# Kernel tuning notes

Measured on AMD Instinct MI355X. Metric: run time of the kernel, lower is better.

The kernel has to match this reference:

```python
import jax, jax.numpy as jnp
import numpy as np

EPS = 1e-5
THRESH = 1.5


def _compute_one(x, g_w, g_b, phi_w, phi_b, W_w, W_b, gamma, beta):
    # x: (c, w, h, z) -- single sample (torch code calls compute_x with batch 1)
    c, w, h, z = x.shape
    nz = z // 2
    # AdaptiveAvgPool3d(1) on x.permute(0,4,2,3,1): mean over (w, h, c) per z-slice -> (z,)
    p = x.mean(axis=(0, 1, 2))
    xp = x * p[None, None, None, :]
    # 1x1x1 conv projections (note: self.theta is defined but unused in the original)
    g_x = jnp.einsum('ic,cwhz->iwhz', g_w, x) + g_b[:, None, None, None]
    phi_x = jnp.einsum('ic,cwhz->iwhz', phi_w, xp) + phi_b[:, None, None, None]
    # MaxPool3d kernel (1,1,2): non-overlapping max pairs along z
    g_x = g_x.reshape(-1, w, h, nz, 2).max(axis=-1)      # (ic, w, h, nz)
    phi_x = phi_x.reshape(-1, w, h, nz, 2).max(axis=-1)  # (ic, w, h, nz)
    # theta_x: (x*p).permute(0,2,3,4,1).view(w*h, z, c)
    theta = xp.transpose(1, 2, 3, 0).reshape(w * h, z, c)
    # phi: permute(0,2,3,1,4).view(w*h, ic, nz)
    phi_m = phi_x.transpose(1, 2, 0, 3).reshape(w * h, -1, nz)
    # g: permute(0,2,3,4,1).view(w*h, nz, ic)
    g_m = g_x.transpose(1, 2, 3, 0).reshape(w * h, nz, -1)
    f = jnp.einsum('bzc,bcn->bzn', theta, phi_m)          # (wh, z, nz)
    a = jax.nn.softmax(f, axis=-1)
    y = jnp.einsum('bzn,bni->bzi', a, g_m)                # (wh, z, ic)
    y = y.reshape(w, h, z, -1).transpose(3, 0, 1, 2)      # (ic, w, h, z)
    wy = jnp.einsum('ci,iwhz->cwhz', W_w, y) + W_b[:, None, None, None]
    # BatchNorm3d in training mode on a single-sample batch: per-channel stats over (w,h,z)
    mu = wy.mean(axis=(1, 2, 3), keepdims=True)
    var = wy.var(axis=(1, 2, 3), keepdims=True)
    wy = (wy - mu) * jax.lax.rsqrt(var + EPS)
    wy = wy * gamma[:, None, None, None] + beta[:, None, None, None]
    return wy + x


def setup_inputs() -> dict:
    key = jax.random.key(0)
    ks = jax.random.split(key, 10)
    b, c, w, h, z = 2, 64, 64, 64, 64
    ic = c  # inter_channels defaults to in_channels
    x = jax.random.normal(ks[0], (b, c, w, h, z), dtype=jnp.float32)
    # spacings in [0, 3): some samples fall above spacing_thresh=1.5 (identity branch)
    spacings = jax.random.uniform(ks[1], (b, 3), dtype=jnp.float32) * 3.0
    g_w = jax.random.normal(ks[2], (ic, c), dtype=jnp.float32) * 0.1
    g_b = jax.random.normal(ks[3], (ic,), dtype=jnp.float32) * 0.1
    phi_w = jax.random.normal(ks[4], (ic, c), dtype=jnp.float32) * 0.1
    phi_b = jax.random.normal(ks[5], (ic,), dtype=jnp.float32) * 0.1
    W_w = jax.random.normal(ks[6], (c, ic), dtype=jnp.float32) * 0.1
    W_b = jax.random.normal(ks[7], (c,), dtype=jnp.float32) * 0.1
    gamma = jax.random.normal(ks[8], (c,), dtype=jnp.float32) * 0.1
    beta = jax.random.normal(ks[9], (c,), dtype=jnp.float32) * 0.1
    return {"x": x, "spacings": spacings, "g_w": g_w, "g_b": g_b,
            "phi_w": phi_w, "phi_b": phi_b, "W_w": W_w, "W_b": W_b,
            "gamma": gamma, "beta": beta}


def reference(x, spacings, g_w, g_b, phi_w, phi_b, W_w, W_b, gamma, beta):
    out = jax.vmap(_compute_one, in_axes=(0,) + (None,) * 8)(
        x, g_w, g_b, phi_w, phi_b, W_w, W_b, gamma, beta)
    use = (spacings[:, -1] <= THRESH)[:, None, None, None, None]
    return jnp.where(use, out, x)
```

## Files before the change

kernel.cpp:

```cpp
#include <hip/hip_runtime.h>
#include <math.h>

#define THRESH_SP 1.5f
#define WHZc   262144
#define CWHZc  16777216

#define WS_PSUM   0
#define WS_SLOT   128
#define WS_SC     8320
#define WS_SH     8448
#define WS_ZERO_N 8320

typedef __attribute__((ext_vector_type(8))) short bf16x8;
typedef __attribute__((ext_vector_type(4))) float floatx4;

#define MFMA(a, b, c) __builtin_amdgcn_mfma_f32_16x16x32_bf16((a), (b), (c), 0, 0, 0)

__device__ __forceinline__ unsigned short f2b(float f) {
    unsigned int u = __builtin_bit_cast(unsigned int, f);
    return (unsigned short)((u + 0x7FFFu + ((u >> 16) & 1u)) >> 16);
}
__device__ __forceinline__ float b2f(unsigned short h) {
    unsigned int u = ((unsigned int)h) << 16;
    return __builtin_bit_cast(float, u);
}
__device__ __forceinline__ unsigned int scale2(unsigned int u, float pv) {
    unsigned short lo = f2b(b2f((unsigned short)(u & 0xffffu)) * pv);
    unsigned short hi = f2b(b2f((unsigned short)(u >> 16)) * pv);
    return (unsigned int)lo | ((unsigned int)hi << 16);
}
__device__ __forceinline__ bf16x8 ldfrag(const unsigned short* p, int elem_off) {
    return *(const bf16x8*)(p + elem_off);
}

__global__ __launch_bounds__(256) void k_zero(float* __restrict__ ws) {
    int i = blockIdx.x * blockDim.x + threadIdx.x;
    if (i < WS_ZERO_N) ws[i] = 0.0f;
}

__global__ __launch_bounds__(256) void k_pmean(const float* __restrict__ x,
                                               const float* __restrict__ sp,
                                               float* __restrict__ ws) {
    const int b = blockIdx.x >> 9;
    if (sp[b*3 + 2] > THRESH_SP) return;
    const int jb = blockIdx.x & 511;
    __shared__ float s[64];
    const int t = threadIdx.x;
    if (t < 64) s[t] = 0.0f;
    __syncthreads();
    const int idx4 = jb * 256 + t;
    const int z0 = (idx4 & 15) * 4;
    float a0 = 0.f, a1 = 0.f, a2 = 0.f, a3 = 0.f;
    const float* xb = x + (size_t)b * CWHZc;
#pragma unroll 4
    for (int it = 0; it < 32; ++it) {
        const float4 v = *(const float4*)&xb[(size_t)(idx4 + it * 131072) * 4];
        a0 += v.x; a1 += v.y; a2 += v.z; a3 += v.w;
    }
    a0 += __shfl_xor(a0, 16); a0 += __shfl_xor(a0, 32);
    a1 += __shfl_xor(a1, 16); a1 += __shfl_xor(a1, 32);
    a2 += __shfl_xor(a2, 16); a2 += __shfl_xor(a2, 32);
    a3 += __shfl_xor(a3, 16); a3 += __shfl_xor(a3, 32);
    if ((t & 63) < 16) {
        unsafeAtomicAdd(&s[z0 + 0], a0);
        unsafeAtomicAdd(&s[z0 + 1], a1);
        unsafeAtomicAdd(&s[z0 + 2], a2);
        unsafeAtomicAdd(&s[z0 + 3], a3);
    }
    __syncthreads();
    if (t < 64) unsafeAtomicAdd(&ws[WS_PSUM + b * 64 + t], s[t]);
}

__global__ __launch_bounds__(256, 4) void k_main(
    const float* __restrict__ x, const float* __restrict__ sp,
    const float* __restrict__ gw, const float* __restrict__ gb,
    const float* __restrict__ pw, const float* __restrict__ pb,
    const float* __restrict__ Wwp, const float* __restrict__ Wbp,
    float* __restrict__ out, float* __restrict__ ws) {
    const int blk = blockIdx.x;
    const int b = blk >> 12;
    if (sp[b*3 + 2] > THRESH_SP) return;
    const int wh = blk & 4095;
    const int xbase = b * CWHZc + wh * 64;

    __shared__ unsigned short xT[64 * 72];
    __shared__ unsigned short wb[64 * 72];
    __shared__ unsigned short gpT[64 * 40];
    __shared__ unsigned short phpN[32 * 72];
    __shared__ unsigned short aT[64 * 40];
    __shared__ float p_s[64];

    const int t  = threadIdx.x;
    const int l  = t & 63;
    const int lr = l & 15;
    const int lq = l >> 4;
    const int zt = (t >> 6) << 4;

#pragma unroll
    for (int k = 0; k < 4; ++k) {
        const int f = t + (k << 8);
        const int c = f & 63, zq = f >> 6;
        const float4 v = *(const float4*)&x[xbase + c * WHZc + zq * 4];
        xT[(zq*4 + 0)*72 + c] = f2b(v.x);
        xT[(zq*4 + 1)*72 + c] = f2b(v.y);
        xT[(zq*4 + 2)*72 + c] = f2b(v.z);
        xT[(zq*4 + 3)*72 + c] = f2b(v.w);
    }
#pragma unroll
    for (int k = 0; k < 4; ++k) {
        const int f = t + (k << 8);
        const int i = f >> 4, c4 = f & 15;
        const float4 v = *(const float4*)&gw[i*64 + c4*4];
        uint2 pk;
        pk.x = (unsigned int)f2b(v.x) | ((unsigned int)f2b(v.y) << 16);
        pk.y = (unsigned int)f2b(v.z) | ((unsigned int)f2b(v.w) << 16);
        *(uint2*)&wb[i*72 + c4*4] = pk;
    }
    if (t < 64) p_s[t] = ws[WS_PSUM + b*64 + t] * (1.0f / 262144.0f);
    __syncthreads();

    {
        const bf16x8 a0 = ldfrag(xT, (zt + lr)*72 + lq*8);
        const bf16x8 a1 = ldfrag(xT, (zt + lr)*72 + lq*8 + 32);
        const int n0 = (zt >> 1) + lq*2;
#pragma unroll
        for (int ti = 0; ti < 4; ++ti) {
            const int i = ti*16 + lr;
            const float bv = gb[i];
            floatx4 acc = {bv, bv, bv, bv};
            acc = MFMA(a0, ldfrag(wb, i*72 + lq*8), acc);
            acc = MFMA(a1, ldfrag(wb, i*72 + lq*8 + 32), acc);
            unsigned int pk = (unsigned int)f2b(fmaxf(acc[0], acc[1])) |
                              ((unsigned int)f2b(fmaxf(acc[2], acc[3])) << 16);
            *(unsigned int*)&gpT[i*40 + n0] = pk;
        }
    }
    __syncthreads();

    {
        const int r = t & 63, cb = (t >> 6) * 2;
        const float pv = p_s[r];
#pragma unroll
        for (int cc = 0; cc < 2; ++cc) {
            uint4 q = *(uint4*)&xT[r*72 + (cb + cc)*8];
            q.x = scale2(q.x, pv); q.y = scale2(q.y, pv);
            q.z = scale2(q.z, pv); q.w = scale2(q.w, pv);
            *(uint4*)&xT[r*72 + (cb + cc)*8] = q;
        }
#pragma unroll
        for (int k = 0; k < 4; ++k) {
            const int f = t + (k << 8);
            const int i = f >> 4, c4 = f & 15;
            const float4 v = *(const float4*)&pw[i*64 + c4*4];
            uint2 pk;
            pk.x = (unsigned int)f2b(v.x) | ((unsigned int)f2b(v.y) << 16);
            pk.y = (unsigned int)f2b(v.z) | ((unsigned int)f2b(v.w) << 16);
            *(uint2*)&wb[i*72 + c4*4] = pk;
        }
    }
    __syncthreads();

    {
        const bf16x8 a0 = ldfrag(xT, (zt + lr)*72 + lq*8);
        const bf16x8 a1 = ldfrag(xT, (zt + lr)*72 + lq*8 + 32);
        const int n0 = (zt >> 1) + lq*2;
#pragma unroll
        for (int ti = 0; ti < 4; ++ti) {
            const int i = ti*16 + lr;
            const float bv = pb[i];
            floatx4 acc = {bv, bv, bv, bv};
            acc = MFMA(a0, ldfrag(wb, i*72 + lq*8), acc);
            acc = MFMA(a1, ldfrag(wb, i*72 + lq*8 + 32), acc);
            phpN[n0*72 + i]       = f2b(fmaxf(acc[0], acc[1]));
            phpN[(n0 + 1)*72 + i] = f2b(fmaxf(acc[2], acc[3]));
        }
    }
    __syncthreads();

    {
        const bf16x8 a0 = ldfrag(xT, (zt + lr)*72 + lq*8);
        const bf16x8 a1 = ldfrag(xT, (zt + lr)*72 + lq*8 + 32);
        floatx4 f0 = {0.f, 0.f, 0.f, 0.f}, f1 = {0.f, 0.f, 0.f, 0.f};
        f0 = MFMA(a0, ldfrag(phpN, lr*72 + lq*8), f0);
        f0 = MFMA(a1, ldfrag(phpN, lr*72 + lq*8 + 32), f0);
        f1 = MFMA(a0, ldfrag(phpN, (16 + lr)*72 + lq*8), f1);
        f1 = MFMA(a1, ldfrag(phpN, (16 + lr)*72 + lq*8 + 32), f1);
#pragma unroll
        for (int r = 0; r < 4; ++r) {
            float m = fmaxf(f0[r], f1[r]);
            m = fmaxf(m, __shfl_xor(m, 1)); m = fmaxf(m, __shfl_xor(m, 2));
            m = fmaxf(m, __shfl_xor(m, 4)); m = fmaxf(m, __shfl_xor(m, 8));
            const float e0 = __expf(f0[r] - m), e1 = __expf(f1[r] - m);
            float s = e0 + e1;
            s += __shfl_xor(s, 1); s += __shfl_xor(s, 2);
            s += __shfl_xor(s, 4); s += __shfl_xor(s, 8);
            const float inv = 1.0f / s;
            const int z = zt + lq*4 + r;
            aT[z*40 + lr]      = f2b(e0 * inv);
            aT[z*40 + lr + 16] = f2b(e1 * inv);
        }
#pragma unroll
        for (int k = 0; k < 4; ++k) {
            const int f = t + (k << 8);
            const int i = f >> 4, c4 = f & 15;
            const float4 v = *(const float4*)&Wwp[i*64 + c4*4];
            uint2 pk;
            pk.x = (unsigned int)f2b(v.x) | ((unsigned int)f2b(v.y) << 16);
            pk.y = (unsigned int)f2b(v.z) | ((unsigned int)f2b(v.w) << 16);
            *(uint2*)&wb[i*72 + c4*4] = pk;
        }
    }
    __syncthreads();

    {
        float* statsf = (float*)phpN;
        if (t < 128) statsf[t] = 0.0f;
        const bf16x8 av = ldfrag(aT, (zt + lr)*40 + lq*8);
#pragma unroll
        for (int ti = 0; ti < 4; ++ti) {
            floatx4 acc = {0.f, 0.f, 0.f, 0.f};
            acc = MFMA(av, ldfrag(gpT, (ti*16 + lr)*40 + lq*8), acc);
#pragma unroll
            for (int r = 0; r < 4; ++r)
                xT[(zt + lq*4 + r)*72 + ti*16 + lr] = f2b(acc[r]);
        }
    }
    __syncthreads();

    {
        float* statsf = (float*)phpN;
        const bf16x8 a0 = ldfrag(xT, (zt + lr)*72 + lq*8);
        const bf16x8 a1 = ldfrag(xT, (zt + lr)*72 + lq*8 + 32);
#pragma unroll
        for (int ti = 0; ti < 4; ++ti) {
            const int co = ti*16 + lr;
            const float bv = Wbp[co];
            floatx4 acc = {bv, bv, bv, bv};
            acc = MFMA(a0, ldfrag(wb, co*72 + lq*8), acc);
            acc = MFMA(a1, ldfrag(wb, co*72 + lq*8 + 32), acc);
            *(float4*)&out[xbase + co * WHZc + zt + lq*4] = *(float4*)&acc;
            float s1 = acc[0] + acc[1] + acc[2] + acc[3];
            float s2 = acc[0]*acc[0] + acc[1]*acc[1] + acc[2]*acc[2] + acc[3]*acc[3];
            s1 += __shfl_xor(s1, 16); s1 += __shfl_xor(s1, 32);
            s2 += __shfl_xor(s2, 16); s2 += __shfl_xor(s2, 32);
            if (lq == 0) {
                atomicAdd(&statsf[co*2],     s1);
                atomicAdd(&statsf[co*2 + 1], s2);
            }
        }
    }
    __syncthreads();
    {
        const float* statsf = (const float*)phpN;
        if (t < 128) {
            const int slot = blk & 31;
            unsafeAtomicAdd(&ws[WS_SLOT + (slot*2 + b)*128 + t], statsf[t]);
        }
    }
}

__global__ __launch_bounds__(128) void k_stats(const float* __restrict__ gamma,
                                               const float* __restrict__ beta,
                                               float* __restrict__ ws) {
    const int t = threadIdx.x;
    if (t >= 128) return;
    const int b = t >> 6, c = t & 63;
    float S1 = 0.f, S2 = 0.f;
    for (int s = 0; s < 32; s++) {
        S1 += ws[WS_SLOT + ((s * 2 + b) * 64 + c) * 2 + 0];
        S2 += ws[WS_SLOT + ((s * 2 + b) * 64 + c) * 2 + 1];
    }
    const float N = 262144.0f;
    const float mu = S1 / N;
    const float var = fmaxf(S2 / N - mu * mu, 0.0f);
    const float sc = gamma[c] * rsqrtf(var + 1e-5f);
    ws[WS_SC + t] = sc;
    ws[WS_SH + t] = beta[c] - mu * sc;
}

__global__ __launch_bounds__(256) void k_final(const float* __restrict__ x,
                                               const float* __restrict__ sp,
                                               float* __restrict__ out,
                                               const float* __restrict__ ws) {
    const bool use0 = sp[2] <= THRESH_SP;
    const bool use1 = sp[5] <= THRESH_SP;
    const int nf4 = (2 * CWHZc) / 4;
    for (int i4 = blockIdx.x * blockDim.x + threadIdx.x; i4 < nf4;
         i4 += gridDim.x * blockDim.x) {
        const int idx = i4 * 4;
        const int b = idx >> 24;
        const bool use = b ? use1 : use0;
        const float4 xv = *(const float4*)&x[idx];
        float4 ov;
        if (use) {
            const int c = (idx >> 18) & 63;
            const float scv = ws[WS_SC + b * 64 + c];
            const float shv = ws[WS_SH + b * 64 + c];
            const float4 wy = *(const float4*)&out[idx];
            ov.x = wy.x * scv + shv + xv.x;
            ov.y = wy.y * scv + shv + xv.y;
            ov.z = wy.z * scv + shv + xv.z;
            ov.w = wy.w * scv + shv + xv.w;
        } else {
            ov = xv;
        }
        *(float4*)&out[idx] = ov;
    }
}

extern "C" void kernel_launch(void* const* d_in, const int* in_sizes, int n_in,
                              void* d_out, int out_size, void* d_ws, size_t ws_size,
                              hipStream_t stream) {
    const float* x     = (const float*)d_in[0];
    const float* spv   = (const float*)d_in[1];
    const float* gw    = (const float*)d_in[2];
    const float* gb    = (const float*)d_in[3];
    const float* pw    = (const float*)d_in[4];
    const float* pb    = (const float*)d_in[5];
    const float* Ww    = (const float*)d_in[6];
    const float* Wb    = (const float*)d_in[7];
    const float* gamma = (const float*)d_in[8];
    const float* beta  = (const float*)d_in[9];
    float* out = (float*)d_out;
    float* ws  = (float*)d_ws;

    k_zero<<<(WS_ZERO_N + 255) / 256, 256, 0, stream>>>(ws);
    k_pmean<<<1024, 256, 0, stream>>>(x, spv, ws);
    k_main<<<8192, 256, 0, stream>>>(x, spv, gw, gb, pw, pb, Ww, Wb, out, ws);
    k_stats<<<1, 128, 0, stream>>>(gamma, beta, ws);
    k_final<<<2048, 256, 0, stream>>>(x, spv, out, ws);
}
```

Measured before the change: 136.4 us.

## Fold p-scaling into projections, store wy as bf16, merge stats into final kernel

The per-z scaling by p is no longer applied to the x tile in shared memory. It is folded algebraically into the phi projection output and the attention logits, which removes one pass over the tile and one barrier. When the workspace is large enough, the intermediate W·y result is written as bf16 to the workspace instead of fp32 to the output, halving that intermediate traffic at some precision cost. The separate k_stats launch is folded into k_final, where each block recomputes the BN scale and shift in shared memory, adding redundant per-block work in exchange for one fewer launch.

```diff
diff --git a/kernel.cpp b/kernel.cpp
--- a/kernel.cpp
+++ b/kernel.cpp
@@ -7,9 +7,9 @@
 
 #define WS_PSUM   0
 #define WS_SLOT   128
-#define WS_SC     8320
-#define WS_SH     8448
 #define WS_ZERO_N 8320
+#define WS_WY_BYTE 65536
+#define WS_WY_NEED (WS_WY_BYTE + 2u * CWHZc * 2u)
 
 typedef __attribute__((ext_vector_type(8))) short bf16x8;
 typedef __attribute__((ext_vector_type(4))) float floatx4;
@@ -23,11 +23,6 @@
 __device__ __forceinline__ float b2f(unsigned short h) {
     unsigned int u = ((unsigned int)h) << 16;
     return __builtin_bit_cast(float, u);
-}
-__device__ __forceinline__ unsigned int scale2(unsigned int u, float pv) {
-    unsigned short lo = f2b(b2f((unsigned short)(u & 0xffffu)) * pv);
-    unsigned short hi = f2b(b2f((unsigned short)(u >> 16)) * pv);
-    return (unsigned int)lo | ((unsigned int)hi << 16);
 }
 __device__ __forceinline__ bf16x8 ldfrag(const unsigned short* p, int elem_off) {
     return *(const bf16x8*)(p + elem_off);
@@ -76,7 +71,8 @@
     const float* __restrict__ gw, const float* __restrict__ gb,
     const float* __restrict__ pw, const float* __restrict__ pb,
     const float* __restrict__ Wwp, const float* __restrict__ Wbp,
-    float* __restrict__ out, float* __restrict__ ws) {
+    float* __restrict__ out, unsigned short* __restrict__ wy16, int use16,
+    float* __restrict__ ws) {
     const int blk = blockIdx.x;
     const int b = blk >> 12;
     if (sp[b*3 + 2] > THRESH_SP) return;
@@ -119,9 +115,12 @@
     if (t < 64) p_s[t] = ws[WS_PSUM + b*64 + t] * (1.0f / 262144.0f);
     __syncthreads();
 
-    {
-        const bf16x8 a0 = ldfrag(xT, (zt + lr)*72 + lq*8);
-        const bf16x8 a1 = ldfrag(xT, (zt + lr)*72 + lq*8 + 32);
+    const bf16x8 a0 = ldfrag(xT, (zt + lr)*72 + lq*8);
+    const bf16x8 a1 = ldfrag(xT, (zt + lr)*72 + lq*8 + 32);
+    const float pz0 = p_s[zt + lq*4 + 0], pz1 = p_s[zt + lq*4 + 1];
+    const float pz2 = p_s[zt + lq*4 + 2], pz3 = p_s[zt + lq*4 + 3];
+
+    {
         const int n0 = (zt >> 1) + lq*2;
 #pragma unroll
         for (int ti = 0; ti < 4; ++ti) {
@@ -137,60 +136,49 @@
     }
     __syncthreads();
 
-    {
-        const int r = t & 63, cb = (t >> 6) * 2;
-        const float pv = p_s[r];
-#pragma unroll
-        for (int cc = 0; cc < 2; ++cc) {
-            uint4 q = *(uint4*)&xT[r*72 + (cb + cc)*8];
-            q.x = scale2(q.x, pv); q.y = scale2(q.y, pv);
-            q.z = scale2(q.z, pv); q.w = scale2(q.w, pv);
-            *(uint4*)&xT[r*72 + (cb + cc)*8] = q;
-        }
-#pragma unroll
-        for (int k = 0; k < 4; ++k) {
-            const int f = t + (k << 8);
-            const int i = f >> 4, c4 = f & 15;
-            const float4 v = *(const float4*)&pw[i*64 + c4*4];
-            uint2 pk;
-            pk.x = (unsigned int)f2b(v.x) | ((unsigned int)f2b(v.y) << 16);
-            pk.y = (unsigned int)f2b(v.z) | ((unsigned int)f2b(v.w) << 16);
-            *(uint2*)&wb[i*72 + c4*4] = pk;
-        }
-    }
-    __syncthreads();
-
-    {
-        const bf16x8 a0 = ldfrag(xT, (zt + lr)*72 + lq*8);
-        const bf16x8 a1 = ldfrag(xT, (zt + lr)*72 + lq*8 + 32);
+#pragma unroll
+    for (int k = 0; k < 4; ++k) {
+        const int f = t + (k << 8);
+        const int i = f >> 4, c4 = f & 15;
+        const float4 v = *(const float4*)&pw[i*64 + c4*4];
+        uint2 pk;
+        pk.x = (unsigned int)f2b(v.x) | ((unsigned int)f2b(v.y) << 16);
+        pk.y = (unsigned int)f2b(v.z) | ((unsigned int)f2b(v.w) << 16);
+        *(uint2*)&wb[i*72 + c4*4] = pk;
+    }
+    __syncthreads();
+
+    {
         const int n0 = (zt >> 1) + lq*2;
 #pragma unroll
         for (int ti = 0; ti < 4; ++ti) {
             const int i = ti*16 + lr;
-            const float bv = pb[i];
-            floatx4 acc = {bv, bv, bv, bv};
+            floatx4 acc = {0.f, 0.f, 0.f, 0.f};
             acc = MFMA(a0, ldfrag(wb, i*72 + lq*8), acc);
             acc = MFMA(a1, ldfrag(wb, i*72 + lq*8 + 32), acc);
-            phpN[n0*72 + i]       = f2b(fmaxf(acc[0], acc[1]));
-            phpN[(n0 + 1)*72 + i] = f2b(fmaxf(acc[2], acc[3]));
-        }
-    }
-    __syncthreads();
-
-    {
-        const bf16x8 a0 = ldfrag(xT, (zt + lr)*72 + lq*8);
-        const bf16x8 a1 = ldfrag(xT, (zt + lr)*72 + lq*8 + 32);
+            const float bv = pb[i];
+            const float v0 = fmaf(acc[0], pz0, bv), v1 = fmaf(acc[1], pz1, bv);
+            const float v2 = fmaf(acc[2], pz2, bv), v3 = fmaf(acc[3], pz3, bv);
+            phpN[n0*72 + i]       = f2b(fmaxf(v0, v1));
+            phpN[(n0 + 1)*72 + i] = f2b(fmaxf(v2, v3));
+        }
+    }
+    __syncthreads();
+
+    {
         floatx4 f0 = {0.f, 0.f, 0.f, 0.f}, f1 = {0.f, 0.f, 0.f, 0.f};
         f0 = MFMA(a0, ldfrag(phpN, lr*72 + lq*8), f0);
         f0 = MFMA(a1, ldfrag(phpN, lr*72 + lq*8 + 32), f0);
         f1 = MFMA(a0, ldfrag(phpN, (16 + lr)*72 + lq*8), f1);
         f1 = MFMA(a1, ldfrag(phpN, (16 + lr)*72 + lq*8 + 32), f1);
+        const float pz[4] = {pz0, pz1, pz2, pz3};
 #pragma unroll
         for (int r = 0; r < 4; ++r) {
-            float m = fmaxf(f0[r], f1[r]);
+            const float fr0 = f0[r] * pz[r], fr1 = f1[r] * pz[r];
+            float m = fmaxf(fr0, fr1);
             m = fmaxf(m, __shfl_xor(m, 1)); m = fmaxf(m, __shfl_xor(m, 2));
             m = fmaxf(m, __shfl_xor(m, 4)); m = fmaxf(m, __shfl_xor(m, 8));
-            const float e0 = __expf(f0[r] - m), e1 = __expf(f1[r] - m);
+            const float e0 = __expf(fr0 - m), e1 = __expf(fr1 - m);
             float s = e0 + e1;
             s += __shfl_xor(s, 1); s += __shfl_xor(s, 2);
             s += __shfl_xor(s, 4); s += __shfl_xor(s, 8);
@@ -229,16 +217,23 @@
 
     {
         float* statsf = (float*)phpN;
-        const bf16x8 a0 = ldfrag(xT, (zt + lr)*72 + lq*8);
-        const bf16x8 a1 = ldfrag(xT, (zt + lr)*72 + lq*8 + 32);
+        const bf16x8 y0 = ldfrag(xT, (zt + lr)*72 + lq*8);
+        const bf16x8 y1 = ldfrag(xT, (zt + lr)*72 + lq*8 + 32);
 #pragma unroll
         for (int ti = 0; ti < 4; ++ti) {
             const int co = ti*16 + lr;
             const float bv = Wbp[co];
             floatx4 acc = {bv, bv, bv, bv};
-            acc = MFMA(a0, ldfrag(wb, co*72 + lq*8), acc);
-            acc = MFMA(a1, ldfrag(wb, co*72 + lq*8 + 32), acc);
-            *(float4*)&out[xbase + co * WHZc + zt + lq*4] = *(float4*)&acc;
+            acc = MFMA(y0, ldfrag(wb, co*72 + lq*8), acc);
+            acc = MFMA(y1, ldfrag(wb, co*72 + lq*8 + 32), acc);
+            if (use16) {
+                uint2 pk;
+                pk.x = (unsigned int)f2b(acc[0]) | ((unsigned int)f2b(acc[1]) << 16);
+                pk.y = (unsigned int)f2b(acc[2]) | ((unsigned int)f2b(acc[3]) << 16);
+                *(uint2*)&wy16[(size_t)xbase + co * WHZc + zt + lq*4] = pk;
+            } else {
+                *(float4*)&out[xbase + co * WHZc + zt + lq*4] = *(float4*)&acc;
+            }
             float s1 = acc[0] + acc[1] + acc[2] + acc[3];
             float s2 = acc[0]*acc[0] + acc[1]*acc[1] + acc[2]*acc[2] + acc[3]*acc[3];
             s1 += __shfl_xor(s1, 16); s1 += __shfl_xor(s1, 32);
@@ -259,31 +254,33 @@
     }
 }
 
-__global__ __launch_bounds__(128) void k_stats(const float* __restrict__ gamma,
-                                               const float* __restrict__ beta,
-                                               float* __restrict__ ws) {
-    const int t = threadIdx.x;
-    if (t >= 128) return;
-    const int b = t >> 6, c = t & 63;
-    float S1 = 0.f, S2 = 0.f;
-    for (int s = 0; s < 32; s++) {
-        S1 += ws[WS_SLOT + ((s * 2 + b) * 64 + c) * 2 + 0];
-        S2 += ws[WS_SLOT + ((s * 2 + b) * 64 + c) * 2 + 1];
-    }
-    const float N = 262144.0f;
-    const float mu = S1 / N;
-    const float var = fmaxf(S2 / N - mu * mu, 0.0f);
-    const float sc = gamma[c] * rsqrtf(var + 1e-5f);
-    ws[WS_SC + t] = sc;
-    ws[WS_SH + t] = beta[c] - mu * sc;
-}
-
 __global__ __launch_bounds__(256) void k_final(const float* __restrict__ x,
                                                const float* __restrict__ sp,
+                                               const float* __restrict__ gamma,
+                                               const float* __restrict__ beta,
                                                float* __restrict__ out,
+                                               const unsigned short* __restrict__ wy16,
+                                               int use16,
                                                const float* __restrict__ ws) {
     const bool use0 = sp[2] <= THRESH_SP;
     const bool use1 = sp[5] <= THRESH_SP;
+    __shared__ float scf[128], shf[128];
+    if ((use0 || use1) && threadIdx.x < 128) {
+        const int t = threadIdx.x;
+        const int b = t >> 6, c = t & 63;
+        float S1 = 0.f, S2 = 0.f;
+        for (int s = 0; s < 32; s++) {
+            S1 += ws[WS_SLOT + (s*2 + b)*128 + c*2 + 0];
+            S2 += ws[WS_SLOT + (s*2 + b)*128 + c*2 + 1];
+        }
+        const float N = 262144.0f;
+        const float mu = S1 / N;
+        const float var = fmaxf(S2 / N - mu * mu, 0.0f);
+        const float sc = gamma[c] * rsqrtf(var + 1e-5f);
+        scf[t] = sc;
+        shf[t] = beta[c] - mu * sc;
+    }
+    __syncthreads();
     const int nf4 = (2 * CWHZc) / 4;
     for (int i4 = blockIdx.x * blockDim.x + threadIdx.x; i4 < nf4;
          i4 += gridDim.x * blockDim.x) {
@@ -294,13 +291,23 @@
         float4 ov;
         if (use) {
             const int c = (idx >> 18) & 63;
-            const float scv = ws[WS_SC + b * 64 + c];
-            const float shv = ws[WS_SH + b * 64 + c];
-            const float4 wy = *(const float4*)&out[idx];
-            ov.x = wy.x * scv + shv + xv.x;
-            ov.y = wy.y * scv + shv + xv.y;
-            ov.z = wy.z * scv + shv + xv.z;
-            ov.w = wy.w * scv + shv + xv.w;
+            const float scv = scf[b * 64 + c];
+            const float shv = shf[b * 64 + c];
+            float w0, w1, w2, w3;
+            if (use16) {
+                const uint2 q = *(const uint2*)&wy16[idx];
+                w0 = b2f((unsigned short)(q.x & 0xffffu));
+                w1 = b2f((unsigned short)(q.x >> 16));
+                w2 = b2f((unsigned short)(q.y & 0xffffu));
+                w3 = b2f((unsigned short)(q.y >> 16));
+            } else {
+                const float4 wy = *(const float4*)&out[idx];
+                w0 = wy.x; w1 = wy.y; w2 = wy.z; w3 = wy.w;
+            }
+            ov.x = w0 * scv + shv + xv.x;
+            ov.y = w1 * scv + shv + xv.y;
+            ov.z = w2 * scv + shv + xv.z;
+            ov.w = w3 * scv + shv + xv.w;
         } else {
             ov = xv;
         }
@@ -323,10 +330,12 @@
     const float* beta  = (const float*)d_in[9];
     float* out = (float*)d_out;
     float* ws  = (float*)d_ws;
+    const int use16 = (ws_size >= (size_t)WS_WY_NEED) ? 1 : 0;
+    unsigned short* wy16 = (unsigned short*)((char*)d_ws + WS_WY_BYTE);
 
     k_zero<<<(WS_ZERO_N + 255) / 256, 256, 0, stream>>>(ws);
     k_pmean<<<1024, 256, 0, stream>>>(x, spv, ws);
-    k_main<<<8192, 256, 0, stream>>>(x, spv, gw, gb, pw, pb, Ww, Wb, out, ws);
-    k_stats<<<1, 128, 0, stream>>>(gamma, beta, ws);
-    k_final<<<2048, 256, 0, stream>>>(x, spv, out, ws);
-}
+    k_main<<<8192, 256, 0, stream>>>(x, spv, gw, gb, pw, pb, Ww, Wb,
+                                     out, wy16, use16, ws);
+    k_final<<<2048, 256, 0, stream>>>(x, spv, gamma, beta, out, wy16, use16, ws);
+}
```

After: 130.6 us. -4.3%, faster.
